# Kernel tuning notes

Hardware: AMD Instinct MI355X
Metric: run time of the kernel (lower is better)

Reference implementation:

```python
import jax, jax.numpy as jnp
import numpy as np

N_EMB = 1024
HEAD_SIZE = 128

def setup_inputs() -> dict:
    key = jax.random.key(0)
    kx, kq, kk, kv = jax.random.split(key, 4)
    s = 1.0 / np.sqrt(N_EMB)
    return {
        "x": jax.random.normal(kx, (4, 4096, N_EMB), dtype=jnp.float32),
        "Wq": jax.random.normal(kq, (N_EMB, HEAD_SIZE), dtype=jnp.float32) * s,
        "Wk": jax.random.normal(kk, (N_EMB, HEAD_SIZE), dtype=jnp.float32) * s,
        "Wv": jax.random.normal(kv, (N_EMB, HEAD_SIZE), dtype=jnp.float32) * s,
    }

def reference(x, Wq, Wk, Wv) -> jnp.ndarray:
    B, T, C = x.shape
    q = jnp.einsum('btc,cd->btd', x, Wq)  # [B,T,H]
    k = jnp.einsum('btc,cd->btd', x, Wk)
    v = jnp.einsum('btc,cd->btd', x, Wv)
    # NOTE: original scales by sqrt(n_emb), not sqrt(head_size)
    wei = jnp.einsum('btd,bsd->bts', q, k) / jnp.sqrt(jnp.asarray(C, x.dtype))
    causal = jnp.tril(jnp.ones((T, T), dtype=bool))
    wei = jnp.where(causal, wei, -jnp.inf)
    wei = jax.nn.softmax(wei, axis=-1)
    return jnp.einsum('bts,bsd->btd', wei, v)
```

## Files before the change

kernel.cpp:

```cpp
#include <hip/hip_runtime.h>
#include <hip/hip_bf16.h>


#define TSEQ 4096
#define NBATCH 4
#define CEMB 1024
#define HS 128
#define NWORK 136

typedef float  f32x4  __attribute__((ext_vector_type(4)));
typedef float  f32x16 __attribute__((ext_vector_type(16)));
typedef __bf16 bf16x4 __attribute__((ext_vector_type(4)));
typedef __bf16 bf16x8 __attribute__((ext_vector_type(8)));
typedef int    i32x2  __attribute__((ext_vector_type(2)));
typedef int    i32x4  __attribute__((ext_vector_type(4)));

__device__ __forceinline__ __bf16 f2b(float f) { return (__bf16)f; }
__device__ __forceinline__ float fexp2(float f) { return __builtin_amdgcn_exp2f(f); }

typedef const __attribute__((address_space(1))) void* gas_ptr;
typedef __attribute__((address_space(3))) void* las_ptr;
__device__ __forceinline__ void gload16(const void* g, void* l) {
  __builtin_amdgcn_global_load_lds((gas_ptr)g, (las_ptr)l, 16, 0, 0);
}

__global__ void wtrans_kernel(const float* __restrict__ Wq,
                              const float* __restrict__ Wk,
                              const float* __restrict__ Wv,
                              __bf16* __restrict__ Wt) {
  const float* W = (blockIdx.y == 0) ? Wq : (blockIdx.y == 1) ? Wk : Wv;
  int g  = blockIdx.x * 256 + threadIdx.x;
  int n  = g & 127;
  int k0 = (g >> 7) * 8;
  bf16x8 v;
#pragma unroll
  for (int i = 0; i < 8; ++i) v[i] = f2b(W[(size_t)(k0 + i) * HS + n]);
  *(bf16x8*)(Wt + (size_t)blockIdx.y * HS * CEMB + (size_t)n * CEMB + k0) = v;
}

__global__ __launch_bounds__(128)
void proj_kernel(const float* __restrict__ x, const __bf16* __restrict__ Wt,
                 __bf16* __restrict__ qb, __bf16* __restrict__ kb,
                 __bf16* __restrict__ vt) {
  __shared__ __align__(16) __bf16 As[64 * 72];
  __shared__ __align__(16) __bf16 Bs[128 * 72];

  const int tid  = threadIdx.x;
  const int lane = tid & 63;
  const int w    = tid >> 6;
  const int l31  = lane & 31;
  const int half = lane >> 5;

  const int bid   = blockIdx.x;
  const int xcd   = bid & 7;
  const int rest  = bid >> 3;
  const int mat   = rest % 3;
  const int mslab = rest / 3;
  const int m0    = (xcd + 8 * mslab) * 64;
  const __bf16* Wm = Wt + (size_t)mat * HS * CEMB;

  f32x16 acc[2][2];
#pragma unroll
  for (int a = 0; a < 2; ++a)
#pragma unroll
    for (int b = 0; b < 2; ++b)
#pragma unroll
      for (int r = 0; r < 16; ++r) acc[a][b][r] = 0.f;

  const int srow = tid >> 3;
  const int soff = tid & 7;

  f32x4  pa[4][2];
  bf16x8 pb[8];
#pragma unroll
  for (int i = 0; i < 4; ++i) {
    const float* p = x + (size_t)(m0 + srow + 16 * i) * CEMB + soff * 8;
    pa[i][0] = *(const f32x4*)p;
    pa[i][1] = *(const f32x4*)(p + 4);
  }
#pragma unroll
  for (int i = 0; i < 8; ++i)
    pb[i] = *(const bf16x8*)(Wm + (size_t)(srow + 16 * i) * CEMB + soff * 8);

  for (int ks = 0; ks < CEMB; ks += 64) {
    __syncthreads();
#pragma unroll
    for (int i = 0; i < 4; ++i) {
      bf16x8 h;
#pragma unroll
      for (int j = 0; j < 4; ++j) {
        h[j]     = f2b(pa[i][0][j]);
        h[4 + j] = f2b(pa[i][1][j]);
      }
      *(bf16x8*)(As + (srow + 16 * i) * 72 + soff * 8) = h;
    }
#pragma unroll
    for (int i = 0; i < 8; ++i)
      *(bf16x8*)(Bs + (srow + 16 * i) * 72 + soff * 8) = pb[i];
    __syncthreads();
    if (ks + 64 < CEMB) {
#pragma unroll
      for (int i = 0; i < 4; ++i) {
        const float* p = x + (size_t)(m0 + srow + 16 * i) * CEMB + ks + 64 + soff * 8;
        pa[i][0] = *(const f32x4*)p;
        pa[i][1] = *(const f32x4*)(p + 4);
      }
#pragma unroll
      for (int i = 0; i < 8; ++i)
        pb[i] = *(const bf16x8*)(Wm + (size_t)(srow + 16 * i) * CEMB + ks + 64 + soff * 8);
    }
#pragma unroll
    for (int kc = 0; kc < 4; ++kc) {
      bf16x8 af[2], bf[2];
#pragma unroll
      for (int mi = 0; mi < 2; ++mi)
        af[mi] = *(const bf16x8*)(As + (mi * 32 + l31) * 72 + kc * 16 + half * 8);
#pragma unroll
      for (int ni = 0; ni < 2; ++ni)
        bf[ni] = *(const bf16x8*)(Bs + (64 * w + ni * 32 + l31) * 72 + kc * 16 + half * 8);
#pragma unroll
      for (int mi = 0; mi < 2; ++mi)
#pragma unroll
        for (int ni = 0; ni < 2; ++ni)
          acc[mi][ni] = __builtin_amdgcn_mfma_f32_32x32x16_bf16(
              af[mi], bf[ni], acc[mi][ni], 0, 0, 0);
    }
  }

  const float qscale = 1.4426950408889634f / 32.0f;
  if (mat == 0) {
#pragma unroll
    for (int mi = 0; mi < 2; ++mi)
#pragma unroll
      for (int ni = 0; ni < 2; ++ni) {
        int n = 64 * w + ni * 32 + l31;
#pragma unroll
        for (int r = 0; r < 16; ++r) {
          int m = m0 + mi * 32 + (r & 3) + 8 * (r >> 2) + 4 * half;
          qb[(size_t)m * HS + n] = f2b(acc[mi][ni][r] * qscale);
        }
      }
  } else if (mat == 1) {
#pragma unroll
    for (int mi = 0; mi < 2; ++mi)
#pragma unroll
      for (int ni = 0; ni < 2; ++ni) {
        int n = 64 * w + ni * 32 + l31;
#pragma unroll
        for (int r = 0; r < 16; ++r) {
          int m = m0 + mi * 32 + (r & 3) + 8 * (r >> 2) + 4 * half;
          kb[(size_t)m * HS + n] = f2b(acc[mi][ni][r]);
        }
      }
  } else {
    const int bt = m0 >> 12;
#pragma unroll
    for (int mi = 0; mi < 2; ++mi)
#pragma unroll
      for (int ni = 0; ni < 2; ++ni) {
        int n = 64 * w + ni * 32 + l31;
#pragma unroll
        for (int g = 0; g < 4; ++g) {
          bf16x4 pk;
#pragma unroll
          for (int d = 0; d < 4; ++d) pk[d] = f2b(acc[mi][ni][4 * g + d]);
          int tl = ((m0 + mi * 32) & 4095) + 8 * g + 4 * half;
          *(bf16x4*)(vt + ((size_t)bt * HS + n) * TSEQ + tl) = pk;
        }
      }
  }
}

__global__ __launch_bounds__(512)
void attn_kernel(const __bf16* __restrict__ qb, const __bf16* __restrict__ kb,
                 const __bf16* __restrict__ vt,
                 __bf16* __restrict__ Opart, float* __restrict__ Lpart) {
  __shared__ __align__(16) __bf16 Kt[2][64 * 128];
  __shared__ __align__(16) __bf16 Vt[2][128 * 64];

  const int tid   = threadIdx.x;
  const int lane  = tid & 63;
  const int w     = tid >> 6;
  const int l31   = lane & 31;
  const int half  = lane >> 5;
  const int batch = blockIdx.y;
  const int xw    = blockIdx.x;

  int q0 = 0;
  while (q0 < 15 && xw >= (((q0 + 1) * (q0 + 2)) >> 1)) ++q0;
  const int split = xw - ((q0 * (q0 + 1)) >> 1);
  const int it0   = split * 4;
  const int it1   = it0 + 4;

  const int strip0 = q0 * 256 + w * 32;
  const size_t bbase = (size_t)batch * TSEQ;

  bf16x8 qf[8];
  {
    const __bf16* qr = qb + (bbase + strip0 + l31) * HS + half * 8;
#pragma unroll
    for (int kc = 0; kc < 8; ++kc) qf[kc] = *(const bf16x8*)(qr + kc * 16);
  }

  const __bf16* kbb = kb + bbase * HS;
  const __bf16* vbb = vt + (size_t)batch * HS * TSEQ;

  auto stage = [&](int buf, int c0) {
#pragma unroll
    for (int i = 0; i < 2; ++i) {
      int idx  = i * 512 + w * 64 + lane;
      int krow = idx >> 4;
      int kug  = (idx & 15) ^ (krow & 7);
      gload16(kbb + (size_t)(c0 + krow) * HS + kug * 8,
              &Kt[buf][(i * 512 + w * 64) * 8]);
      int d   = idx >> 3;
      int vug = (idx & 7) ^ (d & 7);
      gload16(vbb + (size_t)d * TSEQ + c0 + vug * 8,
              &Vt[buf][(i * 512 + w * 64) * 8]);
    }
  };

  f32x16 o[4];
#pragma unroll
  for (int nt = 0; nt < 4; ++nt)
#pragma unroll
    for (int r = 0; r < 16; ++r) o[nt][r] = 0.f;
  float lsum = 0.f;

  int cur = 0;
  stage(0, it0 * 64);

  for (int it = it0; it < it1; ++it) {
    const int c0 = it * 64;
    asm volatile("s_waitcnt vmcnt(0)" ::: "memory");
    __syncthreads();
    if (it + 1 < it1) stage(cur ^ 1, c0 + 64);

    if (c0 <= strip0 + 31) {
      i32x2 pkt[2][4];
#pragma unroll
      for (int t = 0; t < 2; ++t)
#pragma unroll
        for (int j = 0; j < 4; ++j) pkt[t][j] = (i32x2){0, 0};

#pragma unroll
      for (int t = 0; t < 2; ++t) {
        if (c0 + t * 32 <= strip0 + 31) {
          f32x16 s;
#pragma unroll
          for (int r = 0; r < 16; ++r) s[r] = 0.f;
          __builtin_amdgcn_s_setprio(1);
#pragma unroll
          for (int kc = 0; kc < 8; ++kc) {
            int u = 2 * kc + half;
            bf16x8 kf = *(const bf16x8*)(
                &Kt[cur][(t * 32 + l31) * 128 + ((u ^ (l31 & 7)) * 8)]);
            s = __builtin_amdgcn_mfma_f32_32x32x16_bf16(kf, qf[kc], s, 0, 0, 0);
          }
          __builtin_amdgcn_s_setprio(0);
          if (c0 + t * 32 + 31 > strip0) {
#pragma unroll
            for (int r = 0; r < 16; ++r) {
              int key = c0 + t * 32 + (r & 3) + 8 * (r >> 2) + 4 * half;
              if (key > strip0 + l31) s[r] = -INFINITY;
            }
          }
          float p[16], ps = 0.f;
#pragma unroll
          for (int r = 0; r < 16; ++r) { p[r] = fexp2(s[r]); ps += p[r]; }
          lsum += ps;
#pragma unroll
          for (int j = 0; j < 4; ++j) {
            bf16x4 t4;
#pragma unroll
            for (int d = 0; d < 4; ++d) t4[d] = f2b(p[4 * j + d]);
            pkt[t][j] = __builtin_bit_cast(i32x2, t4);
          }
        }
      }
#pragma unroll
      for (int kk = 0; kk < 4; ++kk) {
        int t = kk >> 1, lo = (kk & 1) * 2;
        i32x2 a = pkt[t][lo], b = pkt[t][lo + 1];
        i32x4 af4;
#if defined(__has_builtin) && __has_builtin(__builtin_amdgcn_permlane32_swap)
        {
          auto r0 = __builtin_amdgcn_permlane32_swap(a.x, b.x, false, false);
          auto r1 = __builtin_amdgcn_permlane32_swap(a.y, b.y, false, false);
          af4.x = r0[0]; af4.y = r1[0]; af4.z = r0[1]; af4.w = r1[1];
        }
#else
        {
          i32x2 ra, rb;
          ra.x = __shfl_xor(a.x, 32); ra.y = __shfl_xor(a.y, 32);
          rb.x = __shfl_xor(b.x, 32); rb.y = __shfl_xor(b.y, 32);
          af4.x = half ? rb.x : a.x;
          af4.y = half ? rb.y : a.y;
          af4.z = half ? b.x  : ra.x;
          af4.w = half ? b.y  : ra.y;
        }
#endif
        bf16x8 af = __builtin_bit_cast(bf16x8, af4);
        __builtin_amdgcn_s_setprio(1);
#pragma unroll
        for (int nt = 0; nt < 4; ++nt) {
          int u = 2 * kk + half;
          bf16x8 vf = *(const bf16x8*)(
              &Vt[cur][(nt * 32 + l31) * 64 + ((u ^ (l31 & 7)) * 8)]);
          o[nt] = __builtin_amdgcn_mfma_f32_32x32x16_bf16(af, vf, o[nt], 0, 0, 0);
        }
        __builtin_amdgcn_s_setprio(0);
      }
    }
    cur ^= 1;
  }

  const size_t widx = (size_t)batch * NWORK + xw;
  __bf16* Op = Opart + widx * (256 * 128);
#pragma unroll
  for (int r = 0; r < 16; ++r) {
    int rloc = w * 32 + 4 * half + (r & 3) + 8 * (r >> 2);
#pragma unroll
    for (int nt = 0; nt < 4; ++nt)
      Op[rloc * 128 + nt * 32 + l31] = f2b(o[nt][r]);
  }
  lsum += __shfl_xor(lsum, 32);
  if (half == 0) Lpart[widx * 256 + w * 32 + l31] = lsum;
}

__global__ __launch_bounds__(256)
void reduce_kernel(const __bf16* __restrict__ Opart, const float* __restrict__ Lpart,
                   float* __restrict__ out) {
  const int batch = blockIdx.y;
  const int rowg  = blockIdx.x * 8 + (threadIdx.x >> 5);
  const int q0 = rowg >> 8;
  const int nsp = q0 + 1;
  const int off = (q0 * (q0 + 1)) >> 1;
  const size_t wbase = (size_t)batch * NWORK + off;
  const int row256 = rowg & 255;
  const int c0 = (threadIdx.x & 31) * 4;

  float l = 0.f;
  for (int s = 0; s < nsp; ++s) l += Lpart[(wbase + s) * 256 + row256];
  const float inv = 1.0f / l;

  const __bf16* op = Opart + wbase * (256 * 128) + row256 * 128 + c0;
  f32x4 a = {0.f, 0.f, 0.f, 0.f};
  for (int s = 0; s < nsp; ++s) {
    bf16x4 v = *(const bf16x4*)(op + (size_t)s * 256 * 128);
#pragma unroll
    for (int j = 0; j < 4; ++j) a[j] += (float)v[j];
  }
  a *= inv;
  *(f32x4*)(out + ((size_t)batch * TSEQ + rowg) * HS + c0) = a;
}

extern "C" void kernel_launch(void* const* d_in, const int* in_sizes, int n_in,
                              void* d_out, int out_size, void* d_ws, size_t ws_size,
                              hipStream_t stream) {
  const float* x  = (const float*)d_in[0];
  const float* Wq = (const float*)d_in[1];
  const float* Wk = (const float*)d_in[2];
  const float* Wv = (const float*)d_in[3];
  float* out = (float*)d_out;

  char* ws = (char*)d_ws;
  __bf16* Wt = (__bf16*)ws;
  __bf16* qb = (__bf16*)(ws + 786432);
  __bf16* kb = (__bf16*)(ws + 786432 + 4194304);
  __bf16* vt = (__bf16*)(ws + 786432 + 2 * 4194304);
  __bf16* Opart = (__bf16*)(ws + 786432 + 3 * 4194304);
  float*  Lpart = (float*)(ws + 786432 + 3 * 4194304 +
                           (size_t)NBATCH * NWORK * 256 * 128 * 2);

  wtrans_kernel<<<dim3(64, 3), 256, 0, stream>>>(Wq, Wk, Wv, Wt);
  proj_kernel<<<dim3(768), 128, 0, stream>>>(x, Wt, qb, kb, vt);
  attn_kernel<<<dim3(NWORK, NBATCH), 512, 0, stream>>>(qb, kb, vt, Opart, Lpart);
  reduce_kernel<<<dim3(512, NBATCH), 256, 0, stream>>>(Opart, Lpart, out);
}
```

Baseline: 168.9 us.

## Split K/V staging waits, use rotation swizzle, and stage output through LDS

The K and V tile loads are split into separate stages with their own waitcnt and barrier points. This lets QK^T compute start once K has arrived while V is still in flight. The LDS swizzle changes from XOR to a rotation scheme, and the V tile is packed so two head-dims share a 128-element row. The epilogue writes the output tile to LDS first and then copies it out with coalesced 16-byte global stores instead of scattered 2-byte stores, at the cost of an extra barrier per iteration and an LDS round-trip.

```diff
diff --git a/kernel.cpp b/kernel.cpp
--- a/kernel.cpp
+++ b/kernel.cpp
@@ -175,8 +175,7 @@
 void attn_kernel(const __bf16* __restrict__ qb, const __bf16* __restrict__ kb,
                  const __bf16* __restrict__ vt,
                  __bf16* __restrict__ Opart, float* __restrict__ Lpart) {
-  __shared__ __align__(16) __bf16 Kt[2][64 * 128];
-  __shared__ __align__(16) __bf16 Vt[2][128 * 64];
+  __shared__ __align__(16) __bf16 S[32768];
 
   const int tid   = threadIdx.x;
   const int lane  = tid & 63;
@@ -205,18 +204,26 @@
   const __bf16* kbb = kb + bbase * HS;
   const __bf16* vbb = vt + (size_t)batch * HS * TSEQ;
 
-  auto stage = [&](int buf, int c0) {
+  auto stageK = [&](int buf, int c0) {
 #pragma unroll
     for (int i = 0; i < 2; ++i) {
-      int idx  = i * 512 + w * 64 + lane;
-      int krow = idx >> 4;
-      int kug  = (idx & 15) ^ (krow & 7);
-      gload16(kbb + (size_t)(c0 + krow) * HS + kug * 8,
-              &Kt[buf][(i * 512 + w * 64) * 8]);
-      int d   = idx >> 3;
-      int vug = (idx & 7) ^ (d & 7);
-      gload16(vbb + (size_t)d * TSEQ + c0 + vug * 8,
-              &Vt[buf][(i * 512 + w * 64) * 8]);
+      int idx = i * 512 + w * 64 + lane;
+      int row = idx >> 4;
+      int su  = ((idx & 15) - row) & 15;
+      gload16(kbb + (size_t)(c0 + row) * HS + su * 8,
+              S + buf * 8192 + (i * 512 + w * 64) * 8);
+    }
+  };
+  auto stageV = [&](int buf, int c0) {
+#pragma unroll
+    for (int i = 0; i < 2; ++i) {
+      int idx = i * 512 + w * 64 + lane;
+      int j   = idx >> 4;
+      int qd  = ((idx & 15) - j) & 15;
+      int d   = 2 * j + (qd >> 3);
+      int u   = qd & 7;
+      gload16(vbb + (size_t)d * TSEQ + c0 + u * 8,
+              S + 16384 + buf * 8192 + (i * 512 + w * 64) * 8);
     }
   };
 
@@ -228,21 +235,25 @@
   float lsum = 0.f;
 
   int cur = 0;
-  stage(0, it0 * 64);
+  stageK(0, it0 * 64);
+  stageV(0, it0 * 64);
 
   for (int it = it0; it < it1; ++it) {
     const int c0 = it * 64;
-    asm volatile("s_waitcnt vmcnt(0)" ::: "memory");
+    const bool more = (it + 1 < it1);
+
+    asm volatile("s_waitcnt vmcnt(2)" ::: "memory");
     __syncthreads();
-    if (it + 1 < it1) stage(cur ^ 1, c0 + 64);
-
-    if (c0 <= strip0 + 31) {
-      i32x2 pkt[2][4];
-#pragma unroll
-      for (int t = 0; t < 2; ++t)
-#pragma unroll
-        for (int j = 0; j < 4; ++j) pkt[t][j] = (i32x2){0, 0};
-
+    if (more) stageK(cur ^ 1, c0 + 64);
+
+    const bool active = (c0 <= strip0 + 31);
+    i32x2 pkt[2][4];
+#pragma unroll
+    for (int t = 0; t < 2; ++t)
+#pragma unroll
+      for (int j = 0; j < 4; ++j) pkt[t][j] = (i32x2){0, 0};
+
+    if (active) {
 #pragma unroll
       for (int t = 0; t < 2; ++t) {
         if (c0 + t * 32 <= strip0 + 31) {
@@ -252,9 +263,9 @@
           __builtin_amdgcn_s_setprio(1);
 #pragma unroll
           for (int kc = 0; kc < 8; ++kc) {
-            int u = 2 * kc + half;
+            int row = t * 32 + l31;
             bf16x8 kf = *(const bf16x8*)(
-                &Kt[cur][(t * 32 + l31) * 128 + ((u ^ (l31 & 7)) * 8)]);
+                S + cur * 8192 + row * 128 + (((2 * kc + half) + row) & 15) * 8);
             s = __builtin_amdgcn_mfma_f32_32x32x16_bf16(kf, qf[kc], s, 0, 0, 0);
           }
           __builtin_amdgcn_s_setprio(0);
@@ -278,6 +289,14 @@
           }
         }
       }
+    }
+
+    if (more) asm volatile("s_waitcnt vmcnt(2)" ::: "memory");
+    else      asm volatile("s_waitcnt vmcnt(0)" ::: "memory");
+    __syncthreads();
+    if (more) stageV(cur ^ 1, c0 + 64);
+
+    if (active) {
 #pragma unroll
       for (int kk = 0; kk < 4; ++kk) {
         int t = kk >> 1, lo = (kk & 1) * 2;
@@ -304,9 +323,11 @@
         __builtin_amdgcn_s_setprio(1);
 #pragma unroll
         for (int nt = 0; nt < 4; ++nt) {
-          int u = 2 * kk + half;
+          int d = nt * 32 + l31;
+          int j = d >> 1;
+          int phys = (((d & 1) * 8 + 2 * kk + half) + j) & 15;
           bf16x8 vf = *(const bf16x8*)(
-              &Vt[cur][(nt * 32 + l31) * 64 + ((u ^ (l31 & 7)) * 8)]);
+              S + 16384 + cur * 8192 + j * 128 + phys * 8);
           o[nt] = __builtin_amdgcn_mfma_f32_32x32x16_bf16(af, vf, o[nt], 0, 0, 0);
         }
         __builtin_amdgcn_s_setprio(0);
@@ -315,14 +336,21 @@
     cur ^= 1;
   }
 
+  __syncthreads();
+  __bf16* stg = S + w * 4096;
+#pragma unroll
+  for (int r = 0; r < 16; ++r) {
+    int srow = 4 * half + (r & 3) + 8 * (r >> 2);
+#pragma unroll
+    for (int nt = 0; nt < 4; ++nt)
+      stg[srow * 128 + nt * 32 + l31] = f2b(o[nt][r]);
+  }
   const size_t widx = (size_t)batch * NWORK + xw;
-  __bf16* Op = Opart + widx * (256 * 128);
-#pragma unroll
-  for (int r = 0; r < 16; ++r) {
-    int rloc = w * 32 + 4 * half + (r & 3) + 8 * (r >> 2);
-#pragma unroll
-    for (int nt = 0; nt < 4; ++nt)
-      Op[rloc * 128 + nt * 32 + l31] = f2b(o[nt][r]);
+  __bf16* Op = Opart + widx * (256 * 128) + w * 32 * 128;
+#pragma unroll
+  for (int i = 0; i < 8; ++i) {
+    bf16x8 vv = *(const bf16x8*)(stg + i * 512 + lane * 8);
+    *(bf16x8*)(Op + i * 512 + lane * 8) = vv;
   }
   lsum += __shfl_xor(lsum, 32);
   if (half == 0) Lpart[widx * 256 + w * 32 + l31] = lsum;
```

After: 170.1 us. About the same (+0.7%).
